# Kernel tuning notes

Measured on AMD Instinct MI355X. Metric: run time of the kernel, lower is better.

Reference implementation:

```python
import jax, jax.numpy as jnp
import numpy as np

THRESH = 0.01


def _grid_adj(H, W):
    """4-neighbor grid adjacency with self loops, (N,N) float32."""
    N = H * W
    A = np.eye(N, dtype=np.float32)
    idx = np.arange(N).reshape(H, W)
    A[idx[1:, :].ravel(), idx[:-1, :].ravel()] = 1.0   # up neighbor
    A[idx[:-1, :].ravel(), idx[1:, :].ravel()] = 1.0   # down neighbor
    A[idx[:, 1:].ravel(), idx[:, :-1].ravel()] = 1.0   # left neighbor
    A[idx[:, :-1].ravel(), idx[:, 1:].ravel()] = 1.0   # right neighbor
    return jnp.asarray(A)


def setup_inputs() -> dict:
    key = jax.random.key(0)
    kx, k1, k2, k3, k4 = jax.random.split(key, 5)
    B, C, H, W = 8, 256, 48, 48
    scale = 1.0 / np.sqrt(C)  # keep QK^T logits in a sane range
    return {
        "x": jax.random.normal(kx, (B, C, H, W), dtype=jnp.float32),
        "phi_w": jax.random.normal(k1, (C, C), dtype=jnp.float32) * scale,
        "psi_w": jax.random.normal(k2, (C, C), dtype=jnp.float32) * scale,
        "w0_w": jax.random.normal(k3, (C, C), dtype=jnp.float32) * scale,
        "w1_w": jax.random.normal(k4, (C, C), dtype=jnp.float32) * scale,
    }


def reference(x, phi_w, psi_w, w0_w, w1_w):
    B, C, H, W = x.shape
    N = H * W
    A_base = _grid_adj(H, W)                      # (N, N), static
    X = jnp.transpose(x, (0, 2, 3, 1)).reshape(B, N, C)  # (B, N, C)
    Q = jnp.einsum('bnc,dc->bnd', X, phi_w)       # Linear(no bias): X @ W^T
    K = jnp.einsum('bnc,dc->bnd', X, psi_w)
    S = jax.nn.softmax(jnp.einsum('bnd,bmd->bnm', Q, K), axis=2)  # (B,N,N)
    S = jnp.where(S < THRESH, 0.0, S)
    A = A_base[None, :, :] + S                    # (B, N, N)
    diagA = jnp.diagonal(A, axis1=1, axis2=2)     # (B, N)
    m0 = jnp.einsum('bnc,dc->bnd', X * diagA[..., None], w0_w)
    eye = jnp.eye(N, dtype=x.dtype)
    A_off = A * (1.0 - eye)[None, :, :]
    nbr_msg = jnp.einsum('bnm,bmc->bnc', A_off, X)
    m1 = jnp.einsum('bnc,dc->bnd', nbr_msg, w1_w)
    Y = jax.nn.relu(m0 + m1)                      # (B, N, C_out)
    return jnp.transpose(Y.reshape(B, H, W, -1), (0, 3, 1, 2))
```

## Files before the change

### kernel.cpp

```cpp
#include <hip/hip_runtime.h>

#define HWDIM 48
#define NPIX 2304
#define CDIM 256
#define BATCH 8
#define THRESH 0.01f
#define SHIFT 90.0f
#define LISTCAP 104
#define MCHUNK 576

typedef _Float16 f16;
typedef _Float16 f16x8 __attribute__((ext_vector_type(8)));
typedef float f32x4 __attribute__((ext_vector_type(4)));

#define MFMA16(a, b, c) __builtin_amdgcn_mfma_f32_16x16x32_f16(a, b, c, 0, 0, 0)

static __device__ __forceinline__ unsigned short f16bits(f16 v) {
    return __builtin_bit_cast(unsigned short, v);
}
static __device__ __forceinline__ f16 bits2f16(unsigned short u) {
    return __builtin_bit_cast(f16, u);
}

__global__ __launch_bounds__(256) void prep_kernel(const float* __restrict__ x,
                                                   const float* __restrict__ phi,
                                                   const float* __restrict__ psi,
                                                   const float* __restrict__ w0,
                                                   const float* __restrict__ w1,
                                                   f16* __restrict__ Xh,
                                                   f16* __restrict__ wH,
                                                   float* __restrict__ Zbuf,
                                                   int* __restrict__ cnts) {
    if (blockIdx.z == BATCH) {
        int bid = blockIdx.y * gridDim.x + blockIdx.x;
        int t = bid * 256 + threadIdx.x;
        for (int i = t; i < 4 * CDIM * CDIM; i += 576 * 256) {
            const float* src = (i < 65536) ? phi : (i < 131072) ? psi
                               : (i < 196608) ? w0 : w1;
            wH[i] = (f16)src[i & 65535];
        }
        for (int i = t; i < BATCH * NPIX; i += 576 * 256) {
            Zbuf[i] = 0.0f;
            cnts[i] = 0;
        }
        return;
    }
    __shared__ float tile[32][33];
    int b = blockIdx.z;
    int n0 = blockIdx.x * 32, c0 = blockIdx.y * 32;
    int tx = threadIdx.x & 31, ty = threadIdx.x >> 5;
    const float* xb = x + (size_t)b * CDIM * NPIX;
    f16* XhB = Xh + (size_t)b * NPIX * CDIM;
#pragma unroll
    for (int j = 0; j < 4; ++j) {
        int c = c0 + ty + 8 * j;
        tile[ty + 8 * j][tx] = xb[(size_t)c * NPIX + n0 + tx];
    }
    __syncthreads();
#pragma unroll
    for (int j = 0; j < 4; ++j) {
        int n = n0 + ty + 8 * j;
        XhB[(size_t)n * CDIM + c0 + tx] = (f16)tile[tx][ty + 8 * j];
    }
}

__global__ __launch_bounds__(256) void proj_kernel(const f16* __restrict__ Xh,
                                                   const f16* __restrict__ wH,
                                                   f16* __restrict__ Qh,
                                                   f16* __restrict__ Kh) {
    __shared__ f16 ot[64 * 264];
    int bid = blockIdx.x;
    int b = bid & 7;
    int r72 = bid >> 3;
    int z = (r72 >= 36) ? 1 : 0;
    int n0 = (r72 - z * 36) * 64;
    const f16* Wp = wH + (size_t)z * CDIM * CDIM;
    f16* dst = z ? Kh : Qh;
    int tid = threadIdx.x;
    int l = tid & 63, w = tid >> 6;
    int wr = w >> 1, dw = w & 1;
    int lr = l & 15, lg = l >> 4;
    const f16* Xb = Xh + (size_t)b * NPIX * CDIM;

    f32x4 acc[2][8];
#pragma unroll
    for (int rs = 0; rs < 2; ++rs)
#pragma unroll
        for (int dt = 0; dt < 8; ++dt) acc[rs][dt] = {0.f, 0.f, 0.f, 0.f};

#pragma unroll
    for (int ks = 0; ks < 8; ++ks) {
        f16x8 a0 = *(const f16x8*)(Xb + (size_t)(n0 + wr * 32 + lr) * CDIM + ks * 32 + lg * 8);
        f16x8 a1 = *(const f16x8*)(Xb + (size_t)(n0 + wr * 32 + 16 + lr) * CDIM + ks * 32 + lg * 8);
#pragma unroll
        for (int dt = 0; dt < 8; ++dt) {
            f16x8 bf = *(const f16x8*)(Wp + (size_t)(dw * 128 + dt * 16 + lr) * CDIM + ks * 32 + lg * 8);
            acc[0][dt] = MFMA16(a0, bf, acc[0][dt]);
            acc[1][dt] = MFMA16(a1, bf, acc[1][dt]);
        }
    }
#pragma unroll
    for (int rs = 0; rs < 2; ++rs)
#pragma unroll
        for (int dt = 0; dt < 8; ++dt)
#pragma unroll
            for (int reg = 0; reg < 4; ++reg)
                ot[(wr * 32 + rs * 16 + lg * 4 + reg) * 264 + dw * 128 + dt * 16 + lr] =
                    (f16)acc[rs][dt][reg];
    __syncthreads();
#pragma unroll
    for (int rep = 0; rep < 8; ++rep) {
        int flat = rep * 256 + tid;
        int r = flat >> 5, seg = flat & 31;
        *(f16x8*)(dst + (size_t)(b * NPIX + n0 + r) * CDIM + seg * 8) =
            *(const f16x8*)(ot + r * 264 + seg * 8);
    }
}

__global__ __launch_bounds__(256) void zpass_kernel(const f16* __restrict__ Qh,
                                                    const f16* __restrict__ Kh,
                                                    float* __restrict__ Zbuf,
                                                    float* __restrict__ ediag) {
    __shared__ f16 Qs[32 * 264];
    __shared__ float zpart[4][32];
    int bid = blockIdx.x;
    int b = bid & 7;
    int r = bid >> 3;
    int n0 = (r >> 2) * 32;
    int mc = r & 3;
    int tid = threadIdx.x;
    int l = tid & 63, cw = tid >> 6;
    int lr = l & 15, lg = l >> 4;
    const f16* Qb = Qh + (size_t)b * NPIX * CDIM;
    const f16* Kb = Kh + (size_t)b * NPIX * CDIM;

#pragma unroll
    for (int rep = 0; rep < 4; ++rep) {
        int idx = rep * 256 + tid;
        int row = idx >> 5, seg = idx & 31;
        *(f16x8*)(Qs + row * 264 + seg * 8) =
            *(const f16x8*)(Qb + (size_t)(n0 + row) * CDIM + seg * 8);
    }
    __syncthreads();

    const f16* kbase = Kb + (size_t)(mc * MCHUNK + cw * 16 + lr) * CDIM + lg * 8;
    float zs[2][4] = {{0.f, 0.f, 0.f, 0.f}, {0.f, 0.f, 0.f, 0.f}};
#pragma unroll 1
    for (int mt = 0; mt < 9; ++mt) {
        const f16* kp = kbase + (size_t)mt * 64 * CDIM;
        f32x4 acc[2] = {{0.f, 0.f, 0.f, 0.f}, {0.f, 0.f, 0.f, 0.f}};
#pragma unroll
        for (int ks = 0; ks < 8; ++ks) {
            f16x8 bf = *(const f16x8*)(kp + ks * 32);
            f16x8 qa0 = *(const f16x8*)(Qs + lr * 264 + ks * 32 + lg * 8);
            f16x8 qa1 = *(const f16x8*)(Qs + (16 + lr) * 264 + ks * 32 + lg * 8);
            acc[0] = MFMA16(qa0, bf, acc[0]);
            acc[1] = MFMA16(qa1, bf, acc[1]);
        }
        int m0 = mc * MCHUNK + mt * 64;
#pragma unroll
        for (int rs = 0; rs < 2; ++rs)
#pragma unroll
            for (int reg = 0; reg < 4; ++reg) {
                int row32 = rs * 16 + lg * 4 + reg;
                float e = __expf(acc[rs][reg] - SHIFT);
                zs[rs][reg] += e;
                if (m0 + cw * 16 + lr == n0 + row32)
                    ediag[b * NPIX + n0 + row32] = e;
            }
    }
#pragma unroll
    for (int rs = 0; rs < 2; ++rs)
#pragma unroll
        for (int reg = 0; reg < 4; ++reg) {
            float v = zs[rs][reg];
            v += __shfl_xor(v, 1);
            v += __shfl_xor(v, 2);
            v += __shfl_xor(v, 4);
            v += __shfl_xor(v, 8);
            zs[rs][reg] = v;
        }
    if (lr == 0)
#pragma unroll
        for (int rs = 0; rs < 2; ++rs)
#pragma unroll
            for (int reg = 0; reg < 4; ++reg)
                zpart[cw][rs * 16 + lg * 4 + reg] = zs[rs][reg];
    __syncthreads();
    if (tid < 32) {
        float Zp = zpart[0][tid] + zpart[1][tid] + zpart[2][tid] + zpart[3][tid];
        atomicAdd(&Zbuf[b * NPIX + n0 + tid], Zp);
    }
}

__global__ __launch_bounds__(256) void filter_kernel(const f16* __restrict__ Qh,
                                                     const f16* __restrict__ Kh,
                                                     const float* __restrict__ Zbuf,
                                                     const float* __restrict__ ediag,
                                                     float* __restrict__ diagT,
                                                     unsigned* __restrict__ lists,
                                                     int* __restrict__ cnts) {
    __shared__ f16 Qs[32 * 264];
    __shared__ float invZ_s[32];
    __shared__ float thr_s[32];
    int bid = blockIdx.x;
    int b = bid & 7;
    int r = bid >> 3;
    int n0 = (r >> 2) * 32;
    int mc = r & 3;
    int tid = threadIdx.x;
    int l = tid & 63, cw = tid >> 6;
    int lr = l & 15, lg = l >> 4;
    const f16* Qb = Qh + (size_t)b * NPIX * CDIM;
    const f16* Kb = Kh + (size_t)b * NPIX * CDIM;

#pragma unroll
    for (int rep = 0; rep < 4; ++rep) {
        int idx = rep * 256 + tid;
        int row = idx >> 5, seg = idx & 31;
        *(f16x8*)(Qs + row * 264 + seg * 8) =
            *(const f16x8*)(Qb + (size_t)(n0 + row) * CDIM + seg * 8);
    }
    if (tid < 32) {
        int n = b * NPIX + n0 + tid;
        float Z = Zbuf[n];
        float iz = 1.0f / Z;
        invZ_s[tid] = iz;
        thr_s[tid] = logf(THRESH) + logf(Z) - 1e-3f;
        if (mc == 0) {
            float d = ediag[n] * iz;
            diagT[n] = (d < THRESH) ? 0.0f : d;
        }
    }
    __syncthreads();

    float thrv[2][4], izv[2][4];
#pragma unroll
    for (int rs = 0; rs < 2; ++rs)
#pragma unroll
        for (int reg = 0; reg < 4; ++reg) {
            int row32 = rs * 16 + lg * 4 + reg;
            thrv[rs][reg] = thr_s[row32];
            izv[rs][reg] = invZ_s[row32];
        }

    const f16* kbase = Kb + (size_t)(mc * MCHUNK + cw * 16 + lr) * CDIM + lg * 8;
#pragma unroll 1
    for (int mt = 0; mt < 9; ++mt) {
        const f16* kp = kbase + (size_t)mt * 64 * CDIM;
        f32x4 acc[2] = {{0.f, 0.f, 0.f, 0.f}, {0.f, 0.f, 0.f, 0.f}};
#pragma unroll
        for (int ks = 0; ks < 8; ++ks) {
            f16x8 bf = *(const f16x8*)(kp + ks * 32);
            f16x8 qa0 = *(const f16x8*)(Qs + lr * 264 + ks * 32 + lg * 8);
            f16x8 qa1 = *(const f16x8*)(Qs + (16 + lr) * 264 + ks * 32 + lg * 8);
            acc[0] = MFMA16(qa0, bf, acc[0]);
            acc[1] = MFMA16(qa1, bf, acc[1]);
        }
        int m0 = mc * MCHUNK + mt * 64;
#pragma unroll
        for (int rs = 0; rs < 2; ++rs)
#pragma unroll
            for (int reg = 0; reg < 4; ++reg) {
                float lm = acc[rs][reg] - SHIFT;
                if (lm >= thrv[rs][reg]) {
                    float s = __expf(lm) * izv[rs][reg];
                    if (s >= THRESH) {
                        int row32 = rs * 16 + lg * 4 + reg;
                        int n = b * NPIX + n0 + row32;
                        int idx = atomicAdd(&cnts[n], 1);
                        if (idx < LISTCAP)
                            lists[(size_t)n * LISTCAP + idx] =
                                ((unsigned)(m0 + cw * 16 + lr) << 16) | f16bits((f16)s);
                    }
                }
            }
    }
}

__global__ __launch_bounds__(256) void sparse_kernel(const unsigned* __restrict__ lists,
                                                     const int* __restrict__ cnts,
                                                     const f16* __restrict__ Xh,
                                                     const float* __restrict__ diagT,
                                                     f16* __restrict__ nbrH) {
    int bid = blockIdx.x;
    int b = bid & 7;
    int n0 = (bid >> 3) * 32;
    int tid = threadIdx.x;
    int r = tid >> 3, t8 = tid & 7;
    int n = n0 + r;
    const f16* Xb = Xh + (size_t)b * NPIX * CDIM;
    int k = cnts[b * NPIX + n];
    if (k > LISTCAP) k = LISTCAP;
    const unsigned* lrow = lists + (size_t)(b * NPIX + n) * LISTCAP;

    float accv[32];
#pragma unroll
    for (int j = 0; j < 32; ++j) accv[j] = 0.f;

    auto addrow = [&](int m, float s) {
        const f16* xr = Xb + (size_t)m * CDIM + t8 * 32;
#pragma unroll
        for (int v4 = 0; v4 < 4; ++v4) {
            f16x8 xv = *(const f16x8*)(xr + v4 * 8);
#pragma unroll
            for (int j = 0; j < 8; ++j) accv[v4 * 8 + j] += s * (float)xv[j];
        }
    };

    int hh = n / HWDIM, ww = n % HWDIM;
    if (hh > 0)         addrow(n - HWDIM, 1.0f);
    if (hh < HWDIM - 1) addrow(n + HWDIM, 1.0f);
    if (ww > 0)         addrow(n - 1, 1.0f);
    if (ww < HWDIM - 1) addrow(n + 1, 1.0f);
    addrow(n, -diagT[b * NPIX + n]);

    for (int i = 0; i < k; ++i) {
        unsigned pk = lrow[i];
        addrow((int)(pk >> 16), (float)bits2f16((unsigned short)(pk & 0xffffu)));
    }

    f16* orow = nbrH + ((size_t)b * NPIX + n) * CDIM + t8 * 32;
#pragma unroll
    for (int v4 = 0; v4 < 4; ++v4) {
        f16x8 ov;
#pragma unroll
        for (int j = 0; j < 8; ++j) ov[j] = (f16)accv[v4 * 8 + j];
        *(f16x8*)(orow + v4 * 8) = ov;
    }
}

__global__ __launch_bounds__(256) void final_kernel(const f16* __restrict__ Xh,
                                                    const f16* __restrict__ nbrH,
                                                    const f16* __restrict__ wH,
                                                    const float* __restrict__ diagT,
                                                    float* __restrict__ out) {
    int bid = blockIdx.x;
    int b = bid & 7;
    int n0 = (bid >> 3) * 64;
    int tid = threadIdx.x;
    int l = tid & 63, w = tid >> 6;
    int wr = w >> 1, dw = w & 1;
    int lr = l & 15, lg = l >> 4;
    const f16* Xb = Xh + (size_t)b * NPIX * CDIM;
    const f16* Nb = nbrH + (size_t)b * NPIX * CDIM;
    const f16* w0H = wH + 2 * CDIM * CDIM;
    const f16* w1H = wH + 3 * CDIM * CDIM;

    f32x4 acc[2][8];
#pragma unroll
    for (int rs = 0; rs < 2; ++rs)
#pragma unroll
        for (int dt = 0; dt < 8; ++dt) acc[rs][dt] = {0.f, 0.f, 0.f, 0.f};

#pragma unroll
    for (int ks = 0; ks < 8; ++ks) {
        f16x8 a0 = *(const f16x8*)(Xb + (size_t)(n0 + wr * 32 + lr) * CDIM + ks * 32 + lg * 8);
        f16x8 a1 = *(const f16x8*)(Xb + (size_t)(n0 + wr * 32 + 16 + lr) * CDIM + ks * 32 + lg * 8);
#pragma unroll
        for (int dt = 0; dt < 8; ++dt) {
            f16x8 bf = *(const f16x8*)(w0H + (size_t)(dw * 128 + dt * 16 + lr) * CDIM + ks * 32 + lg * 8);
            acc[0][dt] = MFMA16(a0, bf, acc[0][dt]);
            acc[1][dt] = MFMA16(a1, bf, acc[1][dt]);
        }
    }
#pragma unroll
    for (int rs = 0; rs < 2; ++rs)
#pragma unroll
        for (int reg = 0; reg < 4; ++reg) {
            int n = n0 + wr * 32 + rs * 16 + lg * 4 + reg;
            float s = 1.0f + diagT[b * NPIX + n];
#pragma unroll
            for (int dt = 0; dt < 8; ++dt) acc[rs][dt][reg] *= s;
        }
#pragma unroll
    for (int ks = 0; ks < 8; ++ks) {
        f16x8 a0 = *(const f16x8*)(Nb + (size_t)(n0 + wr * 32 + lr) * CDIM + ks * 32 + lg * 8);
        f16x8 a1 = *(const f16x8*)(Nb + (size_t)(n0 + wr * 32 + 16 + lr) * CDIM + ks * 32 + lg * 8);
#pragma unroll
        for (int dt = 0; dt < 8; ++dt) {
            f16x8 bf = *(const f16x8*)(w1H + (size_t)(dw * 128 + dt * 16 + lr) * CDIM + ks * 32 + lg * 8);
            acc[0][dt] = MFMA16(a0, bf, acc[0][dt]);
            acc[1][dt] = MFMA16(a1, bf, acc[1][dt]);
        }
    }
#pragma unroll
    for (int rs = 0; rs < 2; ++rs)
#pragma unroll
        for (int dt = 0; dt < 8; ++dt) {
            int d = dw * 128 + dt * 16 + lr;
            int nb_ = n0 + wr * 32 + rs * 16 + lg * 4;
            f32x4 v = acc[rs][dt];
#pragma unroll
            for (int reg = 0; reg < 4; ++reg) v[reg] = fmaxf(v[reg], 0.0f);
            *(f32x4*)(out + ((size_t)b * CDIM + d) * NPIX + nb_) = v;
        }
}

extern "C" void kernel_launch(void* const* d_in, const int* in_sizes, int n_in,
                              void* d_out, int out_size, void* d_ws, size_t ws_size,
                              hipStream_t stream) {
    const float* x   = (const float*)d_in[0];
    const float* phi = (const float*)d_in[1];
    const float* psi = (const float*)d_in[2];
    const float* w0  = (const float*)d_in[3];
    const float* w1  = (const float*)d_in[4];
    float* out = (float*)d_out;

    const size_t BNC = (size_t)BATCH * NPIX * CDIM;
    const size_t BN  = (size_t)BATCH * NPIX;
    char* p = (char*)d_ws;
    auto alloc = [&](size_t bytes) { char* r = p; p += (bytes + 255) & ~(size_t)255; return r; };
    f16*      Xh    = (f16*)alloc(BNC * 2);
    f16*      Qh    = (f16*)alloc(BNC * 2);
    f16*      Kh    = (f16*)alloc(BNC * 2);
    f16*      nbrH  = (f16*)alloc(BNC * 2);
    f16*      wH    = (f16*)alloc((size_t)4 * CDIM * CDIM * 2);
    float*    Zbuf  = (float*)alloc(BN * 4);
    float*    ediag = (float*)alloc(BN * 4);
    float*    diagT = (float*)alloc(BN * 4);
    unsigned* lists = (unsigned*)alloc(BN * LISTCAP * 4);
    int*      cnts  = (int*)alloc(BN * 4);

    prep_kernel<<<dim3(72, 8, 9), 256, 0, stream>>>(x, phi, psi, w0, w1, Xh, wH, Zbuf, cnts);
    proj_kernel<<<dim3(576), 256, 0, stream>>>(Xh, wH, Qh, Kh);
    zpass_kernel<<<dim3(2304), 256, 0, stream>>>(Qh, Kh, Zbuf, ediag);
    filter_kernel<<<dim3(2304), 256, 0, stream>>>(Qh, Kh, Zbuf, ediag, diagT, lists, cnts);
    sparse_kernel<<<dim3(576), 256, 0, stream>>>(lists, cnts, Xh, diagT, nbrH);
    final_kernel<<<dim3(288), 256, 0, stream>>>(Xh, nbrH, wH, diagT, out);
}
```

Measured before the change: 337.6 us.

## Restructure QK passes into 256-column blocks with per-block LDS list staging

The zpass and filter kernels no longer loop over nine 64-column K tiles per block with four chunks per row group. Each block now covers 256 columns, with each wave computing a 32x64 tile in one unrolled pass, and the grid grows from 2304 to 5184 blocks. The filter kernel collects surviving entries in shared-memory lists with shared atomics, then reserves global slots with one atomic per row and copies them out. This aims to raise parallelism and instruction-level overlap and to cut global atomic contention. In exchange it loads the Q tile more often, holds more accumulator registers, and uses more LDS, which may lower occupancy.

```diff
diff --git a/kernel.cpp b/kernel.cpp
--- a/kernel.cpp
+++ b/kernel.cpp
@@ -7,7 +7,6 @@
 #define THRESH 0.01f
 #define SHIFT 90.0f
 #define LISTCAP 104
-#define MCHUNK 576
 
 typedef _Float16 f16;
 typedef _Float16 f16x8 __attribute__((ext_vector_type(8)));
@@ -126,10 +125,10 @@
     int bid = blockIdx.x;
     int b = bid & 7;
     int r = bid >> 3;
-    int n0 = (r >> 2) * 32;
-    int mc = r & 3;
+    int mc = r / 72;
+    int n0 = (r % 72) * 32;
     int tid = threadIdx.x;
-    int l = tid & 63, cw = tid >> 6;
+    int l = tid & 63, w = tid >> 6;
     int lr = l & 15, lg = l >> 4;
     const f16* Qb = Qh + (size_t)b * NPIX * CDIM;
     const f16* Kb = Kh + (size_t)b * NPIX * CDIM;
@@ -143,32 +142,38 @@
     }
     __syncthreads();
 
-    const f16* kbase = Kb + (size_t)(mc * MCHUNK + cw * 16 + lr) * CDIM + lg * 8;
+    int m0 = (mc * 4 + w) * 64;
+    f32x4 acc[2][4];
+#pragma unroll
+    for (int rs = 0; rs < 2; ++rs)
+#pragma unroll
+        for (int ct = 0; ct < 4; ++ct) acc[rs][ct] = {0.f, 0.f, 0.f, 0.f};
+
+#pragma unroll
+    for (int ks = 0; ks < 8; ++ks) {
+        f16x8 qa0 = *(const f16x8*)(Qs + lr * 264 + ks * 32 + lg * 8);
+        f16x8 qa1 = *(const f16x8*)(Qs + (16 + lr) * 264 + ks * 32 + lg * 8);
+#pragma unroll
+        for (int ct = 0; ct < 4; ++ct) {
+            f16x8 bf = *(const f16x8*)(Kb + (size_t)(m0 + ct * 16 + lr) * CDIM + ks * 32 + lg * 8);
+            acc[0][ct] = MFMA16(qa0, bf, acc[0][ct]);
+            acc[1][ct] = MFMA16(qa1, bf, acc[1][ct]);
+        }
+    }
+
     float zs[2][4] = {{0.f, 0.f, 0.f, 0.f}, {0.f, 0.f, 0.f, 0.f}};
-#pragma unroll 1
-    for (int mt = 0; mt < 9; ++mt) {
-        const f16* kp = kbase + (size_t)mt * 64 * CDIM;
-        f32x4 acc[2] = {{0.f, 0.f, 0.f, 0.f}, {0.f, 0.f, 0.f, 0.f}};
-#pragma unroll
-        for (int ks = 0; ks < 8; ++ks) {
-            f16x8 bf = *(const f16x8*)(kp + ks * 32);
-            f16x8 qa0 = *(const f16x8*)(Qs + lr * 264 + ks * 32 + lg * 8);
-            f16x8 qa1 = *(const f16x8*)(Qs + (16 + lr) * 264 + ks * 32 + lg * 8);
-            acc[0] = MFMA16(qa0, bf, acc[0]);
-            acc[1] = MFMA16(qa1, bf, acc[1]);
-        }
-        int m0 = mc * MCHUNK + mt * 64;
-#pragma unroll
-        for (int rs = 0; rs < 2; ++rs)
+#pragma unroll
+    for (int rs = 0; rs < 2; ++rs)
+#pragma unroll
+        for (int ct = 0; ct < 4; ++ct)
 #pragma unroll
             for (int reg = 0; reg < 4; ++reg) {
                 int row32 = rs * 16 + lg * 4 + reg;
-                float e = __expf(acc[rs][reg] - SHIFT);
+                float e = __expf(acc[rs][ct][reg] - SHIFT);
                 zs[rs][reg] += e;
-                if (m0 + cw * 16 + lr == n0 + row32)
+                if (m0 + ct * 16 + lr == n0 + row32)
                     ediag[b * NPIX + n0 + row32] = e;
             }
-    }
 #pragma unroll
     for (int rs = 0; rs < 2; ++rs)
 #pragma unroll
@@ -185,7 +190,7 @@
         for (int rs = 0; rs < 2; ++rs)
 #pragma unroll
             for (int reg = 0; reg < 4; ++reg)
-                zpart[cw][rs * 16 + lg * 4 + reg] = zs[rs][reg];
+                zpart[w][rs * 16 + lg * 4 + reg] = zs[rs][reg];
     __syncthreads();
     if (tid < 32) {
         float Zp = zpart[0][tid] + zpart[1][tid] + zpart[2][tid] + zpart[3][tid];
@@ -203,17 +208,21 @@
     __shared__ f16 Qs[32 * 264];
     __shared__ float invZ_s[32];
     __shared__ float thr_s[32];
+    __shared__ int cnt_s[32];
+    __shared__ int gbase[32];
+    __shared__ unsigned list_s[32][LISTCAP];
     int bid = blockIdx.x;
     int b = bid & 7;
     int r = bid >> 3;
-    int n0 = (r >> 2) * 32;
-    int mc = r & 3;
+    int mc = r / 72;
+    int n0 = (r % 72) * 32;
     int tid = threadIdx.x;
-    int l = tid & 63, cw = tid >> 6;
+    int l = tid & 63, w = tid >> 6;
     int lr = l & 15, lg = l >> 4;
     const f16* Qb = Qh + (size_t)b * NPIX * CDIM;
     const f16* Kb = Kh + (size_t)b * NPIX * CDIM;
 
+    if (tid < 32) cnt_s[tid] = 0;
 #pragma unroll
     for (int rep = 0; rep < 4; ++rep) {
         int idx = rep * 256 + tid;
@@ -221,60 +230,72 @@
         *(f16x8*)(Qs + row * 264 + seg * 8) =
             *(const f16x8*)(Qb + (size_t)(n0 + row) * CDIM + seg * 8);
     }
-    if (tid < 32) {
-        int n = b * NPIX + n0 + tid;
+    if (tid >= 32 && tid < 64) {
+        int t = tid - 32;
+        int n = b * NPIX + n0 + t;
         float Z = Zbuf[n];
-        float iz = 1.0f / Z;
-        invZ_s[tid] = iz;
-        thr_s[tid] = logf(THRESH) + logf(Z) - 1e-3f;
+        invZ_s[t] = 1.0f / Z;
+        thr_s[t] = logf(THRESH) + logf(Z) - 1e-3f;
         if (mc == 0) {
-            float d = ediag[n] * iz;
+            float d = ediag[n] * invZ_s[t];
             diagT[n] = (d < THRESH) ? 0.0f : d;
         }
     }
     __syncthreads();
 
-    float thrv[2][4], izv[2][4];
-#pragma unroll
-    for (int rs = 0; rs < 2; ++rs)
-#pragma unroll
-        for (int reg = 0; reg < 4; ++reg) {
-            int row32 = rs * 16 + lg * 4 + reg;
-            thrv[rs][reg] = thr_s[row32];
-            izv[rs][reg] = invZ_s[row32];
-        }
-
-    const f16* kbase = Kb + (size_t)(mc * MCHUNK + cw * 16 + lr) * CDIM + lg * 8;
-#pragma unroll 1
-    for (int mt = 0; mt < 9; ++mt) {
-        const f16* kp = kbase + (size_t)mt * 64 * CDIM;
-        f32x4 acc[2] = {{0.f, 0.f, 0.f, 0.f}, {0.f, 0.f, 0.f, 0.f}};
-#pragma unroll
-        for (int ks = 0; ks < 8; ++ks) {
-            f16x8 bf = *(const f16x8*)(kp + ks * 32);
-            f16x8 qa0 = *(const f16x8*)(Qs + lr * 264 + ks * 32 + lg * 8);
-            f16x8 qa1 = *(const f16x8*)(Qs + (16 + lr) * 264 + ks * 32 + lg * 8);
-            acc[0] = MFMA16(qa0, bf, acc[0]);
-            acc[1] = MFMA16(qa1, bf, acc[1]);
-        }
-        int m0 = mc * MCHUNK + mt * 64;
-#pragma unroll
-        for (int rs = 0; rs < 2; ++rs)
+    int m0 = (mc * 4 + w) * 64;
+    f32x4 acc[2][4];
+#pragma unroll
+    for (int rs = 0; rs < 2; ++rs)
+#pragma unroll
+        for (int ct = 0; ct < 4; ++ct) acc[rs][ct] = {0.f, 0.f, 0.f, 0.f};
+
+#pragma unroll
+    for (int ks = 0; ks < 8; ++ks) {
+        f16x8 qa0 = *(const f16x8*)(Qs + lr * 264 + ks * 32 + lg * 8);
+        f16x8 qa1 = *(const f16x8*)(Qs + (16 + lr) * 264 + ks * 32 + lg * 8);
+#pragma unroll
+        for (int ct = 0; ct < 4; ++ct) {
+            f16x8 bf = *(const f16x8*)(Kb + (size_t)(m0 + ct * 16 + lr) * CDIM + ks * 32 + lg * 8);
+            acc[0][ct] = MFMA16(qa0, bf, acc[0][ct]);
+            acc[1][ct] = MFMA16(qa1, bf, acc[1][ct]);
+        }
+    }
+
+#pragma unroll
+    for (int rs = 0; rs < 2; ++rs)
+#pragma unroll
+        for (int ct = 0; ct < 4; ++ct)
 #pragma unroll
             for (int reg = 0; reg < 4; ++reg) {
-                float lm = acc[rs][reg] - SHIFT;
-                if (lm >= thrv[rs][reg]) {
-                    float s = __expf(lm) * izv[rs][reg];
+                int row32 = rs * 16 + lg * 4 + reg;
+                float lm = acc[rs][ct][reg] - SHIFT;
+                if (lm >= thr_s[row32]) {
+                    float s = __expf(lm) * invZ_s[row32];
                     if (s >= THRESH) {
-                        int row32 = rs * 16 + lg * 4 + reg;
-                        int n = b * NPIX + n0 + row32;
-                        int idx = atomicAdd(&cnts[n], 1);
+                        int idx = atomicAdd(&cnt_s[row32], 1);
                         if (idx < LISTCAP)
-                            lists[(size_t)n * LISTCAP + idx] =
-                                ((unsigned)(m0 + cw * 16 + lr) << 16) | f16bits((f16)s);
+                            list_s[row32][idx] =
+                                ((unsigned)(m0 + ct * 16 + lr) << 16) | f16bits((f16)s);
                     }
                 }
             }
+    __syncthreads();
+    if (tid < 32) {
+        int c = cnt_s[tid];
+        if (c > LISTCAP) c = LISTCAP;
+        cnt_s[tid] = c;
+        gbase[tid] = atomicAdd(&cnts[b * NPIX + n0 + tid], c);
+    }
+    __syncthreads();
+    for (int i = tid; i < 32 * LISTCAP; i += 256) {
+        int row = i / LISTCAP, j = i - row * LISTCAP;
+        if (j < cnt_s[row]) {
+            int n = b * NPIX + n0 + row;
+            int dstidx = gbase[row] + j;
+            if (dstidx < LISTCAP)
+                lists[(size_t)n * LISTCAP + dstidx] = list_s[row][j];
+        }
     }
 }
 
@@ -424,8 +445,8 @@
 
     prep_kernel<<<dim3(72, 8, 9), 256, 0, stream>>>(x, phi, psi, w0, w1, Xh, wH, Zbuf, cnts);
     proj_kernel<<<dim3(576), 256, 0, stream>>>(Xh, wH, Qh, Kh);
-    zpass_kernel<<<dim3(2304), 256, 0, stream>>>(Qh, Kh, Zbuf, ediag);
-    filter_kernel<<<dim3(2304), 256, 0, stream>>>(Qh, Kh, Zbuf, ediag, diagT, lists, cnts);
+    zpass_kernel<<<dim3(5184), 256, 0, stream>>>(Qh, Kh, Zbuf, ediag);
+    filter_kernel<<<dim3(5184), 256, 0, stream>>>(Qh, Kh, Zbuf, ediag, diagT, lists, cnts);
     sparse_kernel<<<dim3(576), 256, 0, stream>>>(lists, cnts, Xh, diagT, nbrH);
     final_kernel<<<dim3(288), 256, 0, stream>>>(Xh, nbrH, wH, diagT, out);
 }
```

Result: faster. 324.2 us (-4.0%).
